# Kernel tuning notes

Measured on AMD Instinct MI355X. Metric: run time of the kernel, lower is better.

## Reference

```python
import jax, jax.numpy as jnp
import numpy as np

KN = 4        # kernel_number
K = 3         # kernel size
CIN = 256
COUT = 256
BN_EPS = 1e-5


def _rotation_matrices(thetas):
    """thetas: [b, n] -> rot mats [b, n, 9, 9] (faithful port of _get_rotation_matrix)."""
    b, n = thetas.shape
    t = thetas.reshape(-1)                      # [b*n]
    x = jnp.cos(t); y = jnp.sin(t)
    a = x - y; bxy = x * y; c = x + y
    z = jnp.zeros_like(t); o = jnp.ones_like(t)
    pos = [
        [a, 1 - a, z, z, z, z, z, z, z],
        [z, x - bxy, bxy, z, 1 - c + bxy, y - bxy, z, z, z],
        [z, z, a, z, z, 1 - a, z, z, z],
        [bxy, y - bxy, z, x - bxy, 1 - c + bxy, z, z, z, z],
        [z, z, z, z, o, z, z, z, z],
        [z, z, z, z, 1 - c + bxy, x - bxy, z, y - bxy, bxy],
        [z, z, z, 1 - a, z, z, a, z, z],
        [z, z, z, y - bxy, 1 - c + bxy, z, bxy, x - bxy, z],
        [z, z, z, z, z, z, z, 1 - a, a],
    ]
    neg = [
        [c, z, z, 1 - c, z, z, z, z, z],
        [-bxy, x + bxy, z, bxy - y, 1 - a - bxy, z, z, z, z],
        [z, 1 - c, c, z, z, z, z, z, z],
        [z, z, z, x + bxy, 1 - a - bxy, z, -bxy, bxy - y, z],
        [z, z, z, z, o, z, z, z, z],
        [z, bxy - y, -bxy, z, 1 - a - bxy, x + bxy, z, z, z],
        [z, z, z, z, z, z, c, 1 - c, z],
        [z, z, z, z, 1 - a - bxy, bxy - y, z, x + bxy, -bxy],
        [z, z, z, z, z, 1 - c, z, z, c],
    ]
    P = jnp.stack([jnp.stack(r, 0) for r in pos], 0)    # [9, 9, b*n]
    N = jnp.stack([jnp.stack(r, 0) for r in neg], 0)    # [9, 9, b*n]
    R = jnp.where(t >= 0, P, N)                          # [9, 9, b*n]
    return R.transpose(2, 0, 1).reshape(b, n, K * K, K * K)


def _rotate_weights(weights, lambdas, thetas):
    """weights [n, Cout, Cin, 3, 3], lambdas/thetas [b, n] -> [b*Cout, Cin, 3, 3]."""
    b, n = thetas.shape
    _, Cout, Cin, _, _ = weights.shape
    rot = _rotation_matrices(thetas) * lambdas[:, :, None, None]   # [b, n, 9, 9]
    rot = rot.transpose(0, 2, 1, 3).reshape(b * K * K, n * K * K)  # [b*9, n*9]
    w = weights.transpose(0, 3, 4, 1, 2).reshape(n * K * K, Cout * Cin)
    w = rot @ w                                                    # [b*9, Cout*Cin]
    w = w.reshape(b, K, K, Cout, Cin).transpose(0, 3, 4, 1, 2)
    return w.reshape(b * Cout, Cin, K, K)


def _forward(x, weight, w_lambda, w_theta, bn_gamma, bn_beta, bn_mean, bn_var):
    b, Cin, H, W = x.shape
    Cout = weight.shape[1]
    # routing: GAP -> linear heads (sigmoid for lambdas, softsign*pi for thetas)
    pooled = x.mean(axis=(2, 3))                        # [b, Cin]
    lambdas = jax.nn.sigmoid(pooled @ w_lambda)         # [b, n]
    thetas = jax.nn.soft_sign(pooled @ w_theta) * jnp.pi  # [b, n]
    # per-sample rotated weights + grouped conv (groups = b)
    rw = _rotate_weights(weight, lambdas, thetas)       # [b*Cout, Cin, 3, 3]
    xr = x.reshape(1, b * Cin, H, W)
    out = jax.lax.conv_general_dilated(
        xr, rw, window_strides=(1, 1), padding=((1, 1), (1, 1)),
        dimension_numbers=('NCHW', 'OIHW', 'NCHW'), feature_group_count=b)
    out = out.reshape(b, Cout, H, W)
    # BatchNorm (inference, running stats) + ReLU
    inv = jax.lax.rsqrt(bn_var + BN_EPS)
    out = (out - bn_mean[None, :, None, None]) * (inv * bn_gamma)[None, :, None, None] \
          + bn_beta[None, :, None, None]
    return jax.nn.relu(out)


def setup_inputs() -> dict:
    key = jax.random.key(0)
    ks = jax.random.split(key, 8)
    B, H, W = 16, 64, 64
    x = jax.random.normal(ks[0], (B, CIN, H, W), dtype=jnp.float32)
    fan_in = CIN * K * K
    weight = jax.random.normal(ks[1], (KN, COUT, CIN, K, K), dtype=jnp.float32) * np.sqrt(2.0 / fan_in)
    w_lambda = jax.random.normal(ks[2], (CIN, KN), dtype=jnp.float32) * np.sqrt(2.0 / CIN)
    w_theta = jax.random.normal(ks[3], (CIN, KN), dtype=jnp.float32) * np.sqrt(2.0 / CIN)
    bn_gamma = jax.random.uniform(ks[4], (COUT,), dtype=jnp.float32, minval=0.5, maxval=1.5)
    bn_beta = jax.random.normal(ks[5], (COUT,), dtype=jnp.float32) * 0.1
    bn_mean = jax.random.normal(ks[6], (COUT,), dtype=jnp.float32) * 0.1
    bn_var = jax.random.uniform(ks[7], (COUT,), dtype=jnp.float32, minval=0.5, maxval=1.5)
    return {'x': x, 'weight': weight, 'w_lambda': w_lambda, 'w_theta': w_theta,
            'bn_gamma': bn_gamma, 'bn_beta': bn_beta, 'bn_mean': bn_mean, 'bn_var': bn_var}


def reference(x, weight, w_lambda, w_theta, bn_gamma, bn_beta, bn_mean, bn_var):
    return _forward(x, weight, w_lambda, w_theta, bn_gamma, bn_beta, bn_mean, bn_var)
```

## Files before the change

kernel.cpp:

```cpp
#include <hip/hip_runtime.h>
#include <math.h>

typedef __bf16  bf16x8 __attribute__((ext_vector_type(8)));
typedef float   f32x4  __attribute__((ext_vector_type(4)));

#define GLD_LDS16(dst, src)                                                      \
    __builtin_amdgcn_global_load_lds(                                            \
        (const __attribute__((address_space(1))) unsigned int*)(src),            \
        (__attribute__((address_space(3))) unsigned int*)(dst), 16, 0, 0)

__global__ __launch_bounds__(256) void transpose_kernel(const float* __restrict__ x,
                                                        __bf16* __restrict__ xT) {
    int h = blockIdx.x, b = blockIdx.y;
    int lane = threadIdx.x & 63, wv = threadIdx.x >> 6;
#pragma unroll
    for (int i = 0; i < 8; i++) {
        int cq = i * 4 + wv;
        const float* src = x + (((size_t)(b * 256 + cq * 8) * 64 + h) * 64 + lane);
        bf16x8 o;
#pragma unroll
        for (int j = 0; j < 8; j++) o[j] = (__bf16)src[(size_t)j * 4096];
        *(bf16x8*)(xT + (((size_t)(b * 64 + h) * 64 + lane) * 256 + cq * 8)) = o;
    }
}

__global__ __launch_bounds__(256) void pool_kernel(const float* __restrict__ x,
                                                   float* __restrict__ pooled) {
    int bc = blockIdx.x;
    const float* p = x + (size_t)bc * 4096;
    int t = threadIdx.x;
    float s = 0.f;
#pragma unroll
    for (int i = 0; i < 16; i++) s += p[t + i * 256];
#pragma unroll
    for (int off = 32; off > 0; off >>= 1) s += __shfl_down(s, off, 64);
    __shared__ float red[4];
    if ((t & 63) == 0) red[t >> 6] = s;
    __syncthreads();
    if (t == 0) pooled[bc] = (red[0] + red[1] + red[2] + red[3]) * (1.f / 4096.f);
}

__global__ __launch_bounds__(256) void rotw_kernel(
    const float* __restrict__ weight, const float* __restrict__ pooled,
    const float* __restrict__ w_lambda, const float* __restrict__ w_theta,
    __bf16* __restrict__ rwq) {
    __shared__ __attribute__((aligned(16))) float sl[16][4][9][12];
    __shared__ float wlds[4][2304];
    int co = blockIdx.x;
    int t = threadIdx.x;
#pragma unroll
    for (int n = 0; n < 4; n++) {
        const float* wp = weight + ((size_t)n * 256 + co) * 2304;
        for (int i = t; i < 2304; i += 256) wlds[n][i] = wp[i];
    }
    if (t < 64) {
        int b = t >> 2, n = t & 3;
        float zl = 0.f, zt = 0.f;
        for (int ci = 0; ci < 256; ci++) {
            float p = pooled[b * 256 + ci];
            zl += p * w_lambda[ci * 4 + n];
            zt += p * w_theta[ci * 4 + n];
        }
        float lam = 1.f / (1.f + expf(-zl));
        float th  = 3.14159265358979323846f * (zt / (1.f + fabsf(zt)));
        float xc = cosf(th), ys = sinf(th);
        float a = xc - ys, bb = xc * ys, c = xc + ys;
        float R[9][9];
#pragma unroll
        for (int i = 0; i < 9; i++)
#pragma unroll
            for (int j = 0; j < 9; j++) R[i][j] = 0.f;
        if (th >= 0.f) {
            R[0][0] = a;       R[0][1] = 1 - a;
            R[1][1] = xc - bb; R[1][2] = bb;       R[1][4] = 1 - c + bb; R[1][5] = ys - bb;
            R[2][2] = a;       R[2][5] = 1 - a;
            R[3][0] = bb;      R[3][1] = ys - bb;  R[3][3] = xc - bb;    R[3][4] = 1 - c + bb;
            R[4][4] = 1.f;
            R[5][4] = 1 - c + bb; R[5][5] = xc - bb; R[5][7] = ys - bb;  R[5][8] = bb;
            R[6][3] = 1 - a;   R[6][6] = a;
            R[7][3] = ys - bb; R[7][4] = 1 - c + bb; R[7][6] = bb;       R[7][7] = xc - bb;
            R[8][7] = 1 - a;   R[8][8] = a;
        } else {
            R[0][0] = c;       R[0][3] = 1 - c;
            R[1][0] = -bb;     R[1][1] = xc + bb;  R[1][3] = bb - ys;    R[1][4] = 1 - a - bb;
            R[2][1] = 1 - c;   R[2][2] = c;
            R[3][3] = xc + bb; R[3][4] = 1 - a - bb; R[3][6] = -bb;      R[3][7] = bb - ys;
            R[4][4] = 1.f;
            R[5][1] = bb - ys; R[5][2] = -bb;      R[5][4] = 1 - a - bb; R[5][5] = xc + bb;
            R[6][6] = c;       R[6][7] = 1 - c;
            R[7][4] = 1 - a - bb; R[7][5] = bb - ys; R[7][7] = xc + bb;  R[7][8] = -bb;
            R[8][5] = 1 - c;   R[8][8] = c;
        }
#pragma unroll
        for (int p = 0; p < 9; p++) {
#pragma unroll
            for (int q = 0; q < 9; q++) sl[b][n][p][q] = lam * R[p][q];
            sl[b][n][p][9] = sl[b][n][p][10] = sl[b][n][p][11] = 0.f;
        }
    }
    __syncthreads();
    int ci = t;
    float4 wa[4], wb[4];
    float  wc[4];
#pragma unroll
    for (int n = 0; n < 4; n++) {
        const float* wp = &wlds[n][ci * 9];
        wa[n] = make_float4(wp[0], wp[1], wp[2], wp[3]);
        wb[n] = make_float4(wp[4], wp[5], wp[6], wp[7]);
        wc[n] = wp[8];
    }
    for (int b = 0; b < 16; b++) {
#pragma unroll
        for (int p = 0; p < 9; p++) {
            float s = 0.f;
#pragma unroll
            for (int n = 0; n < 4; n++) {
                float4 sa = *(const float4*)&sl[b][n][p][0];
                float4 sb = *(const float4*)&sl[b][n][p][4];
                float  sc = sl[b][n][p][8];
                s += sa.x * wa[n].x + sa.y * wa[n].y + sa.z * wa[n].z + sa.w * wa[n].w
                   + sb.x * wb[n].x + sb.y * wb[n].y + sb.z * wb[n].z + sb.w * wb[n].w
                   + sc * wc[n];
            }
            rwq[(((size_t)b * 9 + p) * 256 + co) * 256 + ci] = (__bf16)s;
        }
    }
}

__global__ __launch_bounds__(256, 2) void conv_kernel(
    const __bf16* __restrict__ xT, const __bf16* __restrict__ rwq,
    const float* __restrict__ bn_gamma, const float* __restrict__ bn_beta,
    const float* __restrict__ bn_mean,  const float* __restrict__ bn_var,
    float* __restrict__ out) {
    __shared__ __attribute__((aligned(16))) __bf16 xs[10][4][66][8];
    __shared__ __attribute__((aligned(16))) __bf16 as9[9][4][66][8];
    __shared__ float bns[64], bnh[64];

    const int t    = threadIdx.x;
    const int lane = t & 63;
    const int wv   = t >> 6;
    const int l15  = lane & 15;
    const int kq4  = lane >> 4;

    const int lin  = blockIdx.x;
    const int r    = lin & 7;
    const int k    = lin >> 3;
    const int b    = (r << 1) | (k >> 5);
    const int inner = k & 31;
    const int co0  = (inner & 3) << 6;
    const int h0   = (inner >> 2) << 3;

    if (t < 64) {
        float inv = rsqrtf(bn_var[co0 + t] + 1e-5f);
        float sc = bn_gamma[co0 + t] * inv;
        bns[t] = sc;
        bnh[t] = bn_beta[co0 + t] - bn_mean[co0 + t] * sc;
    }

    f32x4 acc[2][4][4];
#pragma unroll
    for (int rr = 0; rr < 2; rr++)
#pragma unroll
        for (int m = 0; m < 4; m++)
#pragma unroll
            for (int n = 0; n < 4; n++) acc[rr][m][n] = (f32x4){0.f, 0.f, 0.f, 0.f};

    const uint4 zero4 = {0u, 0u, 0u, 0u};
    if (t < 40) {
        int rr = t >> 2, kq = t & 3;
        *(uint4*)&xs[rr][kq][0][0]  = zero4;
        *(uint4*)&xs[rr][kq][65][0] = zero4;
    }

    for (int ci0 = 0; ci0 < 256; ci0 += 32) {
        __syncthreads();
#pragma unroll
        for (int u = wv * 10; u < wv * 10 + 10; u++) {
            int rr = u >> 2, kq = u & 3;
            int hh = h0 - 1 + rr;
            if (hh >= 0 && hh < 64) {
                const __bf16* src = xT + (((size_t)(b * 64 + hh) * 64 + lane) * 256 + ci0 + kq * 8);
                GLD_LDS16(&xs[rr][kq][1 + lane][0], src);
            } else {
                *(uint4*)&xs[rr][kq][1 + lane][0] = zero4;
            }
        }
#pragma unroll
        for (int u = wv * 9; u < wv * 9 + 9; u++) {
            int tap = u >> 2, kq = u & 3;
            const __bf16* src = rwq +
                ((((size_t)b * 9 + tap) * 256 + co0 + lane) * 256 + ci0 + kq * 8);
            GLD_LDS16(&as9[tap][kq][lane][0], src);
        }
        __syncthreads();
#pragma unroll
        for (int tap = 0; tap < 9; tap++) {
            const int dh = tap / 3, dw = tap % 3;
            bf16x8 af[4];
#pragma unroll
            for (int m = 0; m < 4; m++)
                af[m] = *(const bf16x8*)&as9[tap][kq4][m * 16 + l15][0];
#pragma unroll
            for (int rr = 0; rr < 2; rr++) {
                const int hl = wv + rr * 4;
#pragma unroll
                for (int nt = 0; nt < 4; nt++) {
                    bf16x8 bfr = *(const bf16x8*)&xs[hl + dh][kq4][nt * 16 + l15 + dw][0];
#pragma unroll
                    for (int m = 0; m < 4; m++)
                        acc[rr][m][nt] = __builtin_amdgcn_mfma_f32_16x16x32_bf16(
                            af[m], bfr, acc[rr][m][nt], 0, 0, 0);
                }
            }
        }
    }

#pragma unroll
    for (int rr = 0; rr < 2; rr++) {
        const int h = h0 + wv + rr * 4;
#pragma unroll
        for (int m = 0; m < 4; m++) {
#pragma unroll
            for (int reg = 0; reg < 4; reg++) {
                int col = m * 16 + kq4 * 4 + reg;
                float sc = bns[col], sh = bnh[col];
                int co = co0 + col;
#pragma unroll
                for (int nt = 0; nt < 4; nt++) {
                    int w = nt * 16 + l15;
                    float v = acc[rr][m][nt][reg] * sc + sh;
                    out[(((size_t)b * 256 + co) * 64 + h) * 64 + w] = v > 0.f ? v : 0.f;
                }
            }
        }
    }
}

extern "C" void kernel_launch(void* const* d_in, const int* in_sizes, int n_in,
                              void* d_out, int out_size, void* d_ws, size_t ws_size,
                              hipStream_t stream) {
    const float* x        = (const float*)d_in[0];
    const float* weight   = (const float*)d_in[1];
    const float* w_lambda = (const float*)d_in[2];
    const float* w_theta  = (const float*)d_in[3];
    const float* bn_gamma = (const float*)d_in[4];
    const float* bn_beta  = (const float*)d_in[5];
    const float* bn_mean  = (const float*)d_in[6];
    const float* bn_var   = (const float*)d_in[7];
    float* out = (float*)d_out;

    char* ws = (char*)d_ws;
    float*  pooled  = (float*)(ws);
    __bf16* xT      = (__bf16*)(ws + 49152);
    __bf16* rwq     = (__bf16*)(ws + 49152 + 33554432);

    transpose_kernel<<<dim3(64, 16), 256, 0, stream>>>(x, xT);
    pool_kernel<<<4096, 256, 0, stream>>>(x, pooled);
    rotw_kernel<<<256, 256, 0, stream>>>(weight, pooled, w_lambda, w_theta, rwq);
    conv_kernel<<<512, 256, 0, stream>>>(xT, rwq,
                                         bn_gamma, bn_beta, bn_mean, bn_var, out);
}
```

Baseline: 271.4 us.

## Double-buffer conv LDS staging, split routing kernel, pool from bf16 transpose

The conv kernel now keeps two LDS buffers, so the next 32-channel chunk loads while MFMAs run on the current one. This halves the barrier count and lowers occupancy to one block per CU, because LDS use doubles. The pool kernel now reads the bf16 transposed tensor with atomics instead of re-reading the fp32 input, which cuts traffic but pools from bf16-rounded values. Routing moves to a tiny single-block kernel, and the weight rotation is split across four batch groups for more parallelism.

```diff
diff --git a/kernel.cpp b/kernel.cpp
--- a/kernel.cpp
+++ b/kernel.cpp
@@ -24,116 +24,112 @@
     }
 }
 
-__global__ __launch_bounds__(256) void pool_kernel(const float* __restrict__ x,
+__global__ __launch_bounds__(256) void pool_kernel(const __bf16* __restrict__ xT,
                                                    float* __restrict__ pooled) {
-    int bc = blockIdx.x;
-    const float* p = x + (size_t)bc * 4096;
+    int pg = blockIdx.x, b = blockIdx.y;
     int t = threadIdx.x;
+    const __bf16* p = xT + ((size_t)b * 4096 + pg * 256) * 256 + t;
     float s = 0.f;
-#pragma unroll
-    for (int i = 0; i < 16; i++) s += p[t + i * 256];
-#pragma unroll
-    for (int off = 32; off > 0; off >>= 1) s += __shfl_down(s, off, 64);
-    __shared__ float red[4];
-    if ((t & 63) == 0) red[t >> 6] = s;
-    __syncthreads();
-    if (t == 0) pooled[bc] = (red[0] + red[1] + red[2] + red[3]) * (1.f / 4096.f);
-}
-
-__global__ __launch_bounds__(256) void rotw_kernel(
-    const float* __restrict__ weight, const float* __restrict__ pooled,
+#pragma unroll 8
+    for (int i = 0; i < 256; i++) s += (float)p[(size_t)i * 256];
+    atomicAdd(&pooled[b * 256 + t], s * (1.f / 4096.f));
+}
+
+__global__ __launch_bounds__(64) void routing_kernel(
+    const float* __restrict__ pooled,
     const float* __restrict__ w_lambda, const float* __restrict__ w_theta,
-    __bf16* __restrict__ rwq) {
-    __shared__ __attribute__((aligned(16))) float sl[16][4][9][12];
+    float* __restrict__ S) {
+    int t = threadIdx.x;
+    int b = t >> 2, n = t & 3;
+    float zl = 0.f, zt = 0.f;
+    for (int ci = 0; ci < 256; ci++) {
+        float p = pooled[b * 256 + ci];
+        zl += p * w_lambda[ci * 4 + n];
+        zt += p * w_theta[ci * 4 + n];
+    }
+    float lam = 1.f / (1.f + expf(-zl));
+    float th  = 3.14159265358979323846f * (zt / (1.f + fabsf(zt)));
+    float xc = cosf(th), ys = sinf(th);
+    float a = xc - ys, bb = xc * ys, c = xc + ys;
+    float R[9][9];
+#pragma unroll
+    for (int i = 0; i < 9; i++)
+#pragma unroll
+        for (int j = 0; j < 9; j++) R[i][j] = 0.f;
+    if (th >= 0.f) {
+        R[0][0] = a;       R[0][1] = 1 - a;
+        R[1][1] = xc - bb; R[1][2] = bb;       R[1][4] = 1 - c + bb; R[1][5] = ys - bb;
+        R[2][2] = a;       R[2][5] = 1 - a;
+        R[3][0] = bb;      R[3][1] = ys - bb;  R[3][3] = xc - bb;    R[3][4] = 1 - c + bb;
+        R[4][4] = 1.f;
+        R[5][4] = 1 - c + bb; R[5][5] = xc - bb; R[5][7] = ys - bb;  R[5][8] = bb;
+        R[6][3] = 1 - a;   R[6][6] = a;
+        R[7][3] = ys - bb; R[7][4] = 1 - c + bb; R[7][6] = bb;       R[7][7] = xc - bb;
+        R[8][7] = 1 - a;   R[8][8] = a;
+    } else {
+        R[0][0] = c;       R[0][3] = 1 - c;
+        R[1][0] = -bb;     R[1][1] = xc + bb;  R[1][3] = bb - ys;    R[1][4] = 1 - a - bb;
+        R[2][1] = 1 - c;   R[2][2] = c;
+        R[3][3] = xc + bb; R[3][4] = 1 - a - bb; R[3][6] = -bb;      R[3][7] = bb - ys;
+        R[4][4] = 1.f;
+        R[5][1] = bb - ys; R[5][2] = -bb;      R[5][4] = 1 - a - bb; R[5][5] = xc + bb;
+        R[6][6] = c;       R[6][7] = 1 - c;
+        R[7][4] = 1 - a - bb; R[7][5] = bb - ys; R[7][7] = xc + bb;  R[7][8] = -bb;
+        R[8][5] = 1 - c;   R[8][8] = c;
+    }
+    float* Sp = S + (b * 4 + n) * 81;
+#pragma unroll
+    for (int p = 0; p < 9; p++)
+#pragma unroll
+        for (int q = 0; q < 9; q++) Sp[p * 9 + q] = lam * R[p][q];
+}
+
+__global__ __launch_bounds__(256) void rotw_kernel(const float* __restrict__ weight,
+                                                   const float* __restrict__ S,
+                                                   __bf16* __restrict__ rwq) {
     __shared__ float wlds[4][2304];
+    __shared__ float sl[4][324];
     int co = blockIdx.x;
+    int bg = blockIdx.y * 4;
     int t = threadIdx.x;
 #pragma unroll
     for (int n = 0; n < 4; n++) {
         const float* wp = weight + ((size_t)n * 256 + co) * 2304;
         for (int i = t; i < 2304; i += 256) wlds[n][i] = wp[i];
     }
-    if (t < 64) {
-        int b = t >> 2, n = t & 3;
-        float zl = 0.f, zt = 0.f;
-        for (int ci = 0; ci < 256; ci++) {
-            float p = pooled[b * 256 + ci];
-            zl += p * w_lambda[ci * 4 + n];
-            zt += p * w_theta[ci * 4 + n];
-        }
-        float lam = 1.f / (1.f + expf(-zl));
-        float th  = 3.14159265358979323846f * (zt / (1.f + fabsf(zt)));
-        float xc = cosf(th), ys = sinf(th);
-        float a = xc - ys, bb = xc * ys, c = xc + ys;
-        float R[9][9];
-#pragma unroll
-        for (int i = 0; i < 9; i++)
-#pragma unroll
-            for (int j = 0; j < 9; j++) R[i][j] = 0.f;
-        if (th >= 0.f) {
-            R[0][0] = a;       R[0][1] = 1 - a;
-            R[1][1] = xc - bb; R[1][2] = bb;       R[1][4] = 1 - c + bb; R[1][5] = ys - bb;
-            R[2][2] = a;       R[2][5] = 1 - a;
-            R[3][0] = bb;      R[3][1] = ys - bb;  R[3][3] = xc - bb;    R[3][4] = 1 - c + bb;
-            R[4][4] = 1.f;
-            R[5][4] = 1 - c + bb; R[5][5] = xc - bb; R[5][7] = ys - bb;  R[5][8] = bb;
-            R[6][3] = 1 - a;   R[6][6] = a;
-            R[7][3] = ys - bb; R[7][4] = 1 - c + bb; R[7][6] = bb;       R[7][7] = xc - bb;
-            R[8][7] = 1 - a;   R[8][8] = a;
-        } else {
-            R[0][0] = c;       R[0][3] = 1 - c;
-            R[1][0] = -bb;     R[1][1] = xc + bb;  R[1][3] = bb - ys;    R[1][4] = 1 - a - bb;
-            R[2][1] = 1 - c;   R[2][2] = c;
-            R[3][3] = xc + bb; R[3][4] = 1 - a - bb; R[3][6] = -bb;      R[3][7] = bb - ys;
-            R[4][4] = 1.f;
-            R[5][1] = bb - ys; R[5][2] = -bb;      R[5][4] = 1 - a - bb; R[5][5] = xc + bb;
-            R[6][6] = c;       R[6][7] = 1 - c;
-            R[7][4] = 1 - a - bb; R[7][5] = bb - ys; R[7][7] = xc + bb;  R[7][8] = -bb;
-            R[8][5] = 1 - c;   R[8][8] = c;
-        }
-#pragma unroll
-        for (int p = 0; p < 9; p++) {
-#pragma unroll
-            for (int q = 0; q < 9; q++) sl[b][n][p][q] = lam * R[p][q];
-            sl[b][n][p][9] = sl[b][n][p][10] = sl[b][n][p][11] = 0.f;
-        }
-    }
+    for (int i = t; i < 4 * 324; i += 256)
+        sl[i / 324][i % 324] = S[(size_t)(bg + i / 324) * 324 + (i % 324)];
     __syncthreads();
     int ci = t;
-    float4 wa[4], wb[4];
-    float  wc[4];
-#pragma unroll
-    for (int n = 0; n < 4; n++) {
-        const float* wp = &wlds[n][ci * 9];
-        wa[n] = make_float4(wp[0], wp[1], wp[2], wp[3]);
-        wb[n] = make_float4(wp[4], wp[5], wp[6], wp[7]);
-        wc[n] = wp[8];
-    }
-    for (int b = 0; b < 16; b++) {
+    float w[4][9];
+#pragma unroll
+    for (int n = 0; n < 4; n++)
+#pragma unroll
+        for (int q = 0; q < 9; q++) w[n][q] = wlds[n][ci * 9 + q];
+#pragma unroll
+    for (int bl = 0; bl < 4; bl++) {
+        int b = bg + bl;
 #pragma unroll
         for (int p = 0; p < 9; p++) {
             float s = 0.f;
 #pragma unroll
             for (int n = 0; n < 4; n++) {
-                float4 sa = *(const float4*)&sl[b][n][p][0];
-                float4 sb = *(const float4*)&sl[b][n][p][4];
-                float  sc = sl[b][n][p][8];
-                s += sa.x * wa[n].x + sa.y * wa[n].y + sa.z * wa[n].z + sa.w * wa[n].w
-                   + sb.x * wb[n].x + sb.y * wb[n].y + sb.z * wb[n].z + sb.w * wb[n].w
-                   + sc * wc[n];
+                const float* sp = &sl[bl][n * 81 + p * 9];
+#pragma unroll
+                for (int q = 0; q < 9; q++) s += sp[q] * w[n][q];
             }
             rwq[(((size_t)b * 9 + p) * 256 + co) * 256 + ci] = (__bf16)s;
         }
     }
 }
 
-__global__ __launch_bounds__(256, 2) void conv_kernel(
+__global__ __launch_bounds__(256, 1) void conv_kernel(
     const __bf16* __restrict__ xT, const __bf16* __restrict__ rwq,
     const float* __restrict__ bn_gamma, const float* __restrict__ bn_beta,
     const float* __restrict__ bn_mean,  const float* __restrict__ bn_var,
     float* __restrict__ out) {
-    __shared__ __attribute__((aligned(16))) __bf16 xs[10][4][66][8];
-    __shared__ __attribute__((aligned(16))) __bf16 as9[9][4][66][8];
+    __shared__ __attribute__((aligned(16))) __bf16 xs[2][10][4][66][8];
+    __shared__ __attribute__((aligned(16))) __bf16 as9[2][9][4][66][8];
     __shared__ float bns[64], bnh[64];
 
     const int t    = threadIdx.x;
@@ -166,23 +162,23 @@
             for (int n = 0; n < 4; n++) acc[rr][m][n] = (f32x4){0.f, 0.f, 0.f, 0.f};
 
     const uint4 zero4 = {0u, 0u, 0u, 0u};
-    if (t < 40) {
-        int rr = t >> 2, kq = t & 3;
-        *(uint4*)&xs[rr][kq][0][0]  = zero4;
-        *(uint4*)&xs[rr][kq][65][0] = zero4;
-    }
-
-    for (int ci0 = 0; ci0 < 256; ci0 += 32) {
-        __syncthreads();
+    if (t < 80) {
+        int bf = t / 40, r2 = t % 40;
+        int rr = r2 >> 2, kq = r2 & 3;
+        *(uint4*)&xs[bf][rr][kq][0][0]  = zero4;
+        *(uint4*)&xs[bf][rr][kq][65][0] = zero4;
+    }
+
+    auto stage = [&](int bf, int ci0) {
 #pragma unroll
         for (int u = wv * 10; u < wv * 10 + 10; u++) {
             int rr = u >> 2, kq = u & 3;
             int hh = h0 - 1 + rr;
             if (hh >= 0 && hh < 64) {
                 const __bf16* src = xT + (((size_t)(b * 64 + hh) * 64 + lane) * 256 + ci0 + kq * 8);
-                GLD_LDS16(&xs[rr][kq][1 + lane][0], src);
+                GLD_LDS16(&xs[bf][rr][kq][1 + lane][0], src);
             } else {
-                *(uint4*)&xs[rr][kq][1 + lane][0] = zero4;
+                *(uint4*)&xs[bf][rr][kq][1 + lane][0] = zero4;
             }
         }
 #pragma unroll
@@ -190,22 +186,28 @@
             int tap = u >> 2, kq = u & 3;
             const __bf16* src = rwq +
                 ((((size_t)b * 9 + tap) * 256 + co0 + lane) * 256 + ci0 + kq * 8);
-            GLD_LDS16(&as9[tap][kq][lane][0], src);
-        }
+            GLD_LDS16(&as9[bf][tap][kq][lane][0], src);
+        }
+    };
+
+    stage(0, 0);
+    for (int c = 0; c < 8; c++) {
         __syncthreads();
+        if (c < 7) stage((c + 1) & 1, (c + 1) * 32);
+        const int bf = c & 1;
 #pragma unroll
         for (int tap = 0; tap < 9; tap++) {
             const int dh = tap / 3, dw = tap % 3;
             bf16x8 af[4];
 #pragma unroll
             for (int m = 0; m < 4; m++)
-                af[m] = *(const bf16x8*)&as9[tap][kq4][m * 16 + l15][0];
+                af[m] = *(const bf16x8*)&as9[bf][tap][kq4][m * 16 + l15][0];
 #pragma unroll
             for (int rr = 0; rr < 2; rr++) {
                 const int hl = wv + rr * 4;
 #pragma unroll
                 for (int nt = 0; nt < 4; nt++) {
-                    bf16x8 bfr = *(const bf16x8*)&xs[hl + dh][kq4][nt * 16 + l15 + dw][0];
+                    bf16x8 bfr = *(const bf16x8*)&xs[bf][hl + dh][kq4][nt * 16 + l15 + dw][0];
 #pragma unroll
                     for (int m = 0; m < 4; m++)
                         acc[rr][m][nt] = __builtin_amdgcn_mfma_f32_16x16x32_bf16(
@@ -251,12 +253,15 @@
 
     char* ws = (char*)d_ws;
     float*  pooled  = (float*)(ws);
+    float*  S       = (float*)(ws + 16384);
     __bf16* xT      = (__bf16*)(ws + 49152);
     __bf16* rwq     = (__bf16*)(ws + 49152 + 33554432);
 
+    hipMemsetAsync(pooled, 0, 4096 * sizeof(float), stream);
     transpose_kernel<<<dim3(64, 16), 256, 0, stream>>>(x, xT);
-    pool_kernel<<<4096, 256, 0, stream>>>(x, pooled);
-    rotw_kernel<<<256, 256, 0, stream>>>(weight, pooled, w_lambda, w_theta, rwq);
+    pool_kernel<<<dim3(16, 16), 256, 0, stream>>>(xT, pooled);
+    routing_kernel<<<1, 64, 0, stream>>>(pooled, w_lambda, w_theta, S);
+    rotw_kernel<<<dim3(256, 4), 256, 0, stream>>>(weight, S, rwq);
     conv_kernel<<<512, 256, 0, stream>>>(xT, rwq,
                                          bn_gamma, bn_beta, bn_mean, bn_var, out);
 }
```

Measured after the change: 315.7 us. +16.4%, slower.
